# Optimization experiments

Hardware: AMD Instinct MI355X
Metric: run time of the kernel (lower is better)

## Reference

```python
import jax, jax.numpy as jnp
import numpy as np

N_NODES = 50000
N_EDGES = 800000
IN_DIM = 16
H1, H2, H3, HFC = 64, 128, 256, 256


def setup_inputs() -> dict:
    key = jax.random.key(0)
    ks = jax.random.split(key, 8)
    w = lambda k, s: jax.random.normal(k, s, dtype=jnp.float32) * 0.05
    return {
        "X": jax.random.normal(ks[0], (N_NODES, IN_DIM), dtype=jnp.float32),
        "edge_index": jax.random.randint(ks[1], (2, N_EDGES), 0, N_NODES, dtype=jnp.int64),
        "W1": w(ks[2], (2 * IN_DIM, H1)), "b1": jnp.zeros((H1,), jnp.float32),
        "W2": w(ks[3], (2 * H1, H2)), "b2": jnp.zeros((H2,), jnp.float32),
        "W3": w(ks[4], (2 * H2, H3)), "b3": jnp.zeros((H3,), jnp.float32),
        "Wf1": w(ks[5], (H3, HFC)), "bf1": jnp.zeros((HFC,), jnp.float32),
        "Wf2": w(ks[6], (HFC, 1)), "bf2": jnp.zeros((1,), jnp.float32),
    }


def edge_conv(x, edge_index, W, b):
    # EdgeConv (DGCNN): msg = ReLU(Linear([x_i, x_j - x_i])), max-aggregate at i
    src, dst = edge_index[0], edge_index[1]
    xi = x[dst]                      # [E, d] target node feats
    xj = x[src]                      # [E, d] source node feats
    msg = jax.nn.relu(jnp.concatenate([xi, xj - xi], axis=-1) @ W + b)  # [E, out]
    agg = jax.ops.segment_max(msg, dst, num_segments=x.shape[0])        # [N, out]
    # nodes with no incoming edge get -inf from segment_max -> zero them
    return jnp.where(jnp.isneginf(agg), 0.0, agg)


def reference(X, edge_index, W1, b1, W2, b2, W3, b3, Wf1, bf1, Wf2, bf2):
    H = edge_conv(X, edge_index, W1, b1)
    H = edge_conv(H, edge_index, W2, b2)
    H = edge_conv(H, edge_index, W3, b3)
    # MLP head (dropout is identity at inference)
    H = jax.nn.relu(H @ Wf1 + bf1)
    out = jax.nn.sigmoid(H @ Wf2 + bf2)
    return out.squeeze(-1)  # [N]
```

## Files before the change

kernel.cpp:

```cpp
#include <hip/hip_runtime.h>
#include <math.h>

#define NN 50000
#define NE 800000

typedef unsigned short ushort_t;
typedef __attribute__((ext_vector_type(8))) short bf16x8;
typedef __attribute__((ext_vector_type(4))) float f32x4;

__device__ inline unsigned short f2bf(float f) {
    unsigned int u = __float_as_uint(f);
    u = (u + 0x7fffu + ((u >> 16) & 1u)) >> 16;
    return (unsigned short)u;
}
__device__ inline unsigned int pack2bf(float lo, float hi) {
    return (unsigned int)f2bf(lo) | ((unsigned int)f2bf(hi) << 16);
}

__global__ void prep0_kernel(const int* __restrict__ ei, int istride,
                             int* __restrict__ esrc32, int* __restrict__ edst32,
                             int* __restrict__ deg) {
    int i = blockIdx.x * blockDim.x + threadIdx.x;
    int s = gridDim.x * blockDim.x;
    for (int j = i; j < NN; j += s) deg[j] = 0;
    const int* eis = ei;
    const int* eid = ei + (size_t)NE * istride;
    for (int j = i; j < NE; j += s) {
        esrc32[j] = eis[(size_t)j * istride];
        edst32[j] = eid[(size_t)j * istride];
    }
}

__global__ void hist_kernel(const int* __restrict__ edst, int* __restrict__ deg, int nE) {
    int i = blockIdx.x * blockDim.x + threadIdx.x;
    int s = gridDim.x * blockDim.x;
    for (; i < nE; i += s) atomicAdd(&deg[edst[i]], 1);
}

__global__ __launch_bounds__(256)
void scan_reduce(const int* __restrict__ deg, int* __restrict__ bsum, int n) {
    __shared__ int s[256];
    const int t = threadIdx.x;
    const int i = blockIdx.x * 256 + t;
    s[t] = (i < n) ? deg[i] : 0;
    __syncthreads();
#pragma unroll
    for (int off = 128; off > 0; off >>= 1) {
        if (t < off) s[t] += s[t + off];
        __syncthreads();
    }
    if (t == 0) bsum[blockIdx.x] = s[0];
}

__global__ __launch_bounds__(256)
void scan_tops(const int* __restrict__ bsum, int* __restrict__ boff,
               int* __restrict__ rowptr, int nb, int n) {
    __shared__ int s[256];
    const int t = threadIdx.x;
    const int v = (t < nb) ? bsum[t] : 0;
    s[t] = v;
    __syncthreads();
    for (int off = 1; off < 256; off <<= 1) {
        int u = (t >= off) ? s[t - off] : 0;
        __syncthreads();
        s[t] += u;
        __syncthreads();
    }
    if (t < nb) boff[t] = s[t] - v;
    if (t == 255) rowptr[n] = s[255];
}

__global__ __launch_bounds__(256)
void scan_apply(int* __restrict__ deg, const int* __restrict__ boff,
                int* __restrict__ rowptr, int n) {
    __shared__ int s[256];
    const int t = threadIdx.x;
    const int i = blockIdx.x * 256 + t;
    const int v = (i < n) ? deg[i] : 0;
    s[t] = v;
    __syncthreads();
    for (int off = 1; off < 256; off <<= 1) {
        int u = (t >= off) ? s[t - off] : 0;
        __syncthreads();
        s[t] += u;
        __syncthreads();
    }
    if (i < n) {
        int ex = boff[blockIdx.x] + s[t] - v;
        rowptr[i] = ex;
        deg[i] = ex;
    }
}

__global__ void scatter_kernel(const int* __restrict__ esrc, const int* __restrict__ edst,
                               int* __restrict__ cursor, int* __restrict__ col, int nE) {
    int i = blockIdx.x * blockDim.x + threadIdx.x;
    int s = gridDim.x * blockDim.x;
    for (; i < nE; i += s) {
        int d = edst[i];
        int pos = atomicAdd(&cursor[d], 1);
        col[pos] = esrc[i];
    }
}

__global__ void megaprep_kernel(const float* __restrict__ W1, const float* __restrict__ W2,
                                const float* __restrict__ W3, const float* __restrict__ Wf1,
                                const float* __restrict__ X,
                                ushort_t* __restrict__ Wt1, ushort_t* __restrict__ Wt2,
                                ushort_t* __restrict__ Wt3, ushort_t* __restrict__ Wf1t,
                                ushort_t* __restrict__ Xb, float* __restrict__ hacc) {
    const int T0 = 128 * 32;
    const int T1 = T0 + 256 * 64;
    const int T2 = T1 + 512 * 128;
    const int T3 = T2 + 256 * 256;
    const int T4 = T3 + NN * 32;
    const int T5 = T4 + NN;
    int i = blockIdx.x * blockDim.x + threadIdx.x;
    int s = gridDim.x * blockDim.x;
    for (; i < T5; i += s) {
        if (i < T0) {
            int idx = i, o = idx / 32, k = idx % 32;
            float v = 0.f;
            if (k < 16)
                v = (o < 64) ? (W1[k * 64 + o] - W1[(k + 16) * 64 + o])
                             : W1[(k + 16) * 64 + (o - 64)];
            Wt1[idx] = f2bf(v);
        } else if (i < T1) {
            int idx = i - T0, o = idx / 64, k = idx % 64;
            float v = (o < 128) ? (W2[k * 128 + o] - W2[(k + 64) * 128 + o])
                                : W2[(k + 64) * 128 + (o - 128)];
            Wt2[idx] = f2bf(v);
        } else if (i < T2) {
            int idx = i - T1, o = idx / 128, k = idx % 128;
            float v = (o < 256) ? (W3[(size_t)k * 256 + o] - W3[(size_t)(k + 128) * 256 + o])
                                : W3[(size_t)(k + 128) * 256 + (o - 256)];
            Wt3[idx] = f2bf(v);
        } else if (i < T3) {
            int idx = i - T2, nn = idx / 256, k = idx % 256;
            Wf1t[idx] = f2bf(Wf1[(size_t)k * 256 + nn]);
        } else if (i < T4) {
            int idx = i - T3, row = idx >> 5, c = idx & 31;
            Xb[idx] = (c < 16) ? f2bf(X[(size_t)row * 16 + c]) : (ushort_t)0;
        } else {
            hacc[i - T4] = 0.f;
        }
    }
}

template<int K, int OUT, int NF, int MR>
__global__ __launch_bounds__(256, 3)
void gemm_mfma(const ushort_t* __restrict__ A, const ushort_t* __restrict__ Wt,
               const float* __restrict__ bias, ushort_t* __restrict__ PQ, int n) {
    constexpr int NOUT = 2 * OUT;
    constexpr int KB = K / 32;
    __shared__ ushort_t lds[128][132];

    const int wave = threadIdx.x >> 6;
    const int lane = threadIdx.x & 63;
    const int lr = lane & 15;
    const int kg = lane >> 4;
    const int row0b = blockIdx.x * (4 * MR * 16);
    const int row0 = row0b + wave * (MR * 16);
    const int col0 = blockIdx.y * (NF * 16);

    f32x4 acc[MR][NF];
#pragma unroll
    for (int m = 0; m < MR; ++m)
#pragma unroll
        for (int f = 0; f < NF; ++f) acc[m][f] = (f32x4)(0.f);

    const ushort_t* Ap[MR];
#pragma unroll
    for (int m = 0; m < MR; ++m) {
        int arow = row0 + m * 16 + lr;
        if (arow >= n) arow = n - 1;
        Ap[m] = A + (size_t)arow * K + kg * 8;
    }
    const ushort_t* Bp = Wt + (size_t)(col0 + lr) * K + kg * 8;

    bf16x8 af[2][MR];
    bf16x8 bfv[2][NF];
#pragma unroll
    for (int m = 0; m < MR; ++m) af[0][m] = *(const bf16x8*)(Ap[m]);
#pragma unroll
    for (int f = 0; f < NF; ++f) bfv[0][f] = *(const bf16x8*)(Bp + (size_t)f * 16 * K);

#pragma unroll
    for (int kb = 0; kb < KB; ++kb) {
        const int cur = kb & 1, nxt = cur ^ 1;
        if (kb + 1 < KB) {
#pragma unroll
            for (int m = 0; m < MR; ++m)
                af[nxt][m] = *(const bf16x8*)(Ap[m] + (kb + 1) * 32);
#pragma unroll
            for (int f = 0; f < NF; ++f)
                bfv[nxt][f] = *(const bf16x8*)(Bp + (size_t)f * 16 * K + (kb + 1) * 32);
        }
#pragma unroll
        for (int f = 0; f < NF; ++f)
#pragma unroll
            for (int m = 0; m < MR; ++m)
                acc[m][f] = __builtin_amdgcn_mfma_f32_16x16x32_bf16(af[cur][m], bfv[cur][f], acc[m][f], 0, 0, 0);
    }

#pragma unroll
    for (int m = 0; m < MR; ++m) {
#pragma unroll
        for (int f = 0; f < NF; ++f) {
            int cg = col0 + f * 16 + lr;
            float bb = (cg < OUT) ? bias[cg] : 0.f;
#pragma unroll
            for (int r = 0; r < 4; ++r) {
                lds[wave * (MR * 16) + m * 16 + kg * 4 + r][f * 16 + lr] =
                    f2bf(acc[m][f][r] + bb);
            }
        }
    }
    __syncthreads();

    const int t = threadIdx.x;
#pragma unroll
    for (int it = 0; it < 8; ++it) {
        int j = it * 256 + t;
        int row = j >> 4;
        int q = j & 15;
        int grow = row0b + row;
        if (grow < n) {
            uint4 v = *(const uint4*)(&lds[row][q * 8]);
            *(uint4*)(PQ + (size_t)grow * NOUT + col0 + q * 8) = v;
        }
    }
}

__global__ __launch_bounds__(256, 3)
void head_mfma(const ushort_t* __restrict__ H, const ushort_t* __restrict__ Wf1t,
               const float* __restrict__ bf1, const float* __restrict__ Wf2,
               float* __restrict__ hacc, int n) {
    __shared__ ushort_t ldsB[64 * 264];

    const int t = threadIdx.x;
    const int wave = t >> 6;
    const int lane = t & 63;
    const int lr = lane & 15;
    const int kg = lane >> 4;
    const int row0 = blockIdx.x * 256 + wave * 64;
    const int col0 = blockIdx.y * 64;

#pragma unroll
    for (int it = 0; it < 8; ++it) {
        int j = it * 256 + t;
        int row = j >> 5;
        int q = j & 31;
        uint4 v = *(const uint4*)(Wf1t + (size_t)(col0 + row) * 256 + q * 8);
        *(uint4*)(&ldsB[row * 264 + q * 8]) = v;
    }
    __syncthreads();

    f32x4 acc[4][4];
#pragma unroll
    for (int m = 0; m < 4; ++m)
#pragma unroll
        for (int f = 0; f < 4; ++f) acc[m][f] = (f32x4)(0.f);

    const ushort_t* Ap[4];
#pragma unroll
    for (int m = 0; m < 4; ++m) {
        int arow = row0 + m * 16 + lr;
        if (arow >= n) arow = n - 1;
        Ap[m] = H + (size_t)arow * 256 + kg * 8;
    }
    const ushort_t* Bl = ldsB + lr * 264 + kg * 8;

#pragma unroll
    for (int kb = 0; kb < 8; ++kb) {
        bf16x8 af[4];
#pragma unroll
        for (int m = 0; m < 4; ++m) af[m] = *(const bf16x8*)(Ap[m] + kb * 32);
        bf16x8 bfv[4];
#pragma unroll
        for (int f = 0; f < 4; ++f)
            bfv[f] = *(const bf16x8*)(Bl + f * 16 * 264 + kb * 32);
#pragma unroll
        for (int f = 0; f < 4; ++f)
#pragma unroll
            for (int m = 0; m < 4; ++m)
                acc[m][f] = __builtin_amdgcn_mfma_f32_16x16x32_bf16(af[m], bfv[f], acc[m][f], 0, 0, 0);
    }

    float part[4][4];
#pragma unroll
    for (int m = 0; m < 4; ++m)
#pragma unroll
        for (int r = 0; r < 4; ++r) part[m][r] = 0.f;

#pragma unroll
    for (int f = 0; f < 4; ++f) {
        int c = col0 + f * 16 + lr;
        float w2 = Wf2[c];
        float bb = bf1[c];
#pragma unroll
        for (int m = 0; m < 4; ++m)
#pragma unroll
            for (int r = 0; r < 4; ++r)
                part[m][r] = fmaf(fmaxf(acc[m][f][r] + bb, 0.f), w2, part[m][r]);
    }
#pragma unroll
    for (int s = 1; s < 16; s <<= 1) {
#pragma unroll
        for (int m = 0; m < 4; ++m)
#pragma unroll
            for (int r = 0; r < 4; ++r)
                part[m][r] += __shfl_xor(part[m][r], s, 16);
    }
    if (lr == 0) {
#pragma unroll
        for (int m = 0; m < 4; ++m)
#pragma unroll
            for (int r = 0; r < 4; ++r) {
                int row = row0 + m * 16 + kg * 4 + r;
                if (row < n) atomicAdd(&hacc[row], part[m][r]);
            }
    }
}

__global__ void sigmoid_kernel(const float* __restrict__ hacc, const float* __restrict__ bf2,
                               float* __restrict__ out, int n) {
    int i = blockIdx.x * blockDim.x + threadIdx.x;
    int s = gridDim.x * blockDim.x;
    float b = bf2[0];
    for (; i < n; i += s) out[i] = 1.f / (1.f + expf(-(hacc[i] + b)));
}

template<int OUT>
__global__ __launch_bounds__(256, 8)
void segmax_combine(const ushort_t* __restrict__ PQ, const int* __restrict__ rowptr,
                    const int* __restrict__ col, ushort_t* __restrict__ Hout, int n) {
    constexpr int NOUT = 2 * OUT;
    constexpr int G = OUT / 8;
    constexpr int NPB = 256 / G;
    const int gid = threadIdx.x / G;
    const int lane = threadIdx.x % G;
    const int i = blockIdx.x * NPB + gid;
    if (i >= n) return;

    const int r0 = rowptr[i];
    const int r1 = rowptr[i + 1];
    const int c8 = lane * 8;

    float m[8];
#pragma unroll
    for (int j = 0; j < 8; ++j) m[j] = -INFINITY;

    auto domax = [&](uint4 q) {
        m[0] = fmaxf(m[0], __uint_as_float(q.x << 16));
        m[1] = fmaxf(m[1], __uint_as_float(q.x & 0xffff0000u));
        m[2] = fmaxf(m[2], __uint_as_float(q.y << 16));
        m[3] = fmaxf(m[3], __uint_as_float(q.y & 0xffff0000u));
        m[4] = fmaxf(m[4], __uint_as_float(q.z << 16));
        m[5] = fmaxf(m[5], __uint_as_float(q.z & 0xffff0000u));
        m[6] = fmaxf(m[6], __uint_as_float(q.w << 16));
        m[7] = fmaxf(m[7], __uint_as_float(q.w & 0xffff0000u));
    };

    int r = r0;
    for (; r + 3 < r1; r += 4) {
        int s0 = col[r], s1 = col[r + 1], s2 = col[r + 2], s3 = col[r + 3];
        uint4 q0 = *(const uint4*)(PQ + (size_t)s0 * NOUT + OUT + c8);
        uint4 q1 = *(const uint4*)(PQ + (size_t)s1 * NOUT + OUT + c8);
        uint4 q2 = *(const uint4*)(PQ + (size_t)s2 * NOUT + OUT + c8);
        uint4 q3 = *(const uint4*)(PQ + (size_t)s3 * NOUT + OUT + c8);
        domax(q0); domax(q1); domax(q2); domax(q3);
    }
    for (; r < r1; ++r) {
        domax(*(const uint4*)(PQ + (size_t)col[r] * NOUT + OUT + c8));
    }

    const uint4 pb = *(const uint4*)(PQ + (size_t)i * NOUT + c8);
    float p[8];
    p[0] = __uint_as_float(pb.x << 16); p[1] = __uint_as_float(pb.x & 0xffff0000u);
    p[2] = __uint_as_float(pb.y << 16); p[3] = __uint_as_float(pb.y & 0xffff0000u);
    p[4] = __uint_as_float(pb.z << 16); p[5] = __uint_as_float(pb.z & 0xffff0000u);
    p[6] = __uint_as_float(pb.w << 16); p[7] = __uint_as_float(pb.w & 0xffff0000u);

    float h[8];
#pragma unroll
    for (int j = 0; j < 8; ++j) h[j] = fmaxf(p[j] + m[j], 0.f);

    uint4 o;
    o.x = pack2bf(h[0], h[1]);
    o.y = pack2bf(h[2], h[3]);
    o.z = pack2bf(h[4], h[5]);
    o.w = pack2bf(h[6], h[7]);
    *(uint4*)(Hout + (size_t)i * OUT + c8) = o;
}

extern "C" void kernel_launch(void* const* d_in, const int* in_sizes, int n_in,
                              void* d_out, int out_size, void* d_ws, size_t ws_size,
                              hipStream_t stream) {
    const float* X   = (const float*)d_in[0];
    const int*   ei  = (const int*)d_in[1];
    const float* W1  = (const float*)d_in[2];
    const float* b1  = (const float*)d_in[3];
    const float* W2  = (const float*)d_in[4];
    const float* b2  = (const float*)d_in[5];
    const float* W3  = (const float*)d_in[6];
    const float* b3  = (const float*)d_in[7];
    const float* Wf1 = (const float*)d_in[8];
    const float* bf1 = (const float*)d_in[9];
    const float* Wf2 = (const float*)d_in[10];
    const float* bf2 = (const float*)d_in[11];
    float* out = (float*)d_out;

    int istride = (in_sizes[1] == 4 * NE) ? 2 : 1;

    ushort_t* PQ     = (ushort_t*)d_ws;
    ushort_t* Ha     = PQ + (size_t)NN * 512;
    ushort_t* Hb     = Ha + (size_t)NN * 256;
    int*      rowptr = (int*)(Hb + (size_t)NN * 256);
    int*      deg    = rowptr + (NN + 8);
    int*      col    = deg + NN;
    int*      esrc32 = col + NE;
    int*      edst32 = esrc32 + NE;
    int*      bsum   = edst32 + NE;
    int*      boff   = bsum + 256;
    ushort_t* Wt1    = (ushort_t*)(boff + 256);
    ushort_t* Wt2    = Wt1 + 128 * 32;
    ushort_t* Wt3    = Wt2 + 256 * 64;
    ushort_t* Wf1t   = Wt3 + 512 * 128;
    ushort_t* Xb     = Wf1t + 256 * 256;
    float*    hacc   = (float*)(Xb + (size_t)NN * 32);

    const int NB = (NN + 255) / 256;

    prep0_kernel<<<1024, 256, 0, stream>>>(ei, istride, esrc32, edst32, deg);
    hist_kernel<<<1024, 256, 0, stream>>>(edst32, deg, NE);
    scan_reduce<<<NB, 256, 0, stream>>>(deg, bsum, NN);
    scan_tops<<<1, 256, 0, stream>>>(bsum, boff, rowptr, NB, NN);
    scan_apply<<<NB, 256, 0, stream>>>(deg, boff, rowptr, NN);
    scatter_kernel<<<1024, 256, 0, stream>>>(esrc32, edst32, deg, col, NE);

    megaprep_kernel<<<1024, 256, 0, stream>>>(W1, W2, W3, Wf1, X,
                                              Wt1, Wt2, Wt3, Wf1t, Xb, hacc);

    const int GB = (NN + 127) / 128;

    {
        dim3 g(GB, 1);
        gemm_mfma<32, 64, 8, 2><<<g, 256, 0, stream>>>(Xb, Wt1, b1, PQ, NN);
    }
    segmax_combine<64><<<(NN + 31) / 32, 256, 0, stream>>>(PQ, rowptr, col, Ha, NN);

    {
        dim3 g(GB, 2);
        gemm_mfma<64, 128, 8, 2><<<g, 256, 0, stream>>>(Ha, Wt2, b2, PQ, NN);
    }
    segmax_combine<128><<<(NN + 15) / 16, 256, 0, stream>>>(PQ, rowptr, col, Hb, NN);

    {
        dim3 g(GB, 4);
        gemm_mfma<128, 256, 8, 2><<<g, 256, 0, stream>>>(Hb, Wt3, b3, PQ, NN);
    }
    segmax_combine<256><<<(NN + 7) / 8, 256, 0, stream>>>(PQ, rowptr, col, Ha, NN);

    {
        dim3 g((NN + 255) / 256, 4);
        head_mfma<<<g, 256, 0, stream>>>(Ha, Wf1t, bf1, Wf2, hacc, NN);
    }
    sigmoid_kernel<<<64, 256, 0, stream>>>(hacc, bf2, out, NN);
}
```

Before: 310.2 us.

## Slice segment-max by feature column per XCD and partition CSR scatter by destination

The segment-max kernels now split each node's output features into 8 column slices, with the slice chosen by blockIdx modulo 8. On MI355X's 8 XCDs this means each XCD's L2 sees only one eighth of the PQ row footprint. The CSR scatter also filters edges by destination range per block-modulo-8 partition, so each XCD's atomics hit a disjoint cursor range. The cost is that every node's rowptr/col list is re-read 8 times, each scatter block scans all edges, and this relies on round-robin block-to-XCD dispatch.

```diff
diff --git a/kernel.cpp b/kernel.cpp
--- a/kernel.cpp
+++ b/kernel.cpp
@@ -92,14 +92,20 @@
     }
 }
 
-__global__ void scatter_kernel(const int* __restrict__ esrc, const int* __restrict__ edst,
-                               int* __restrict__ cursor, int* __restrict__ col, int nE) {
-    int i = blockIdx.x * blockDim.x + threadIdx.x;
-    int s = gridDim.x * blockDim.x;
-    for (; i < nE; i += s) {
+__global__ __launch_bounds__(256)
+void scatter_part(const int* __restrict__ esrc, const int* __restrict__ edst,
+                  int* __restrict__ cursor, int* __restrict__ col, int nE) {
+    const int part = blockIdx.x & 7;
+    const int nb = gridDim.x >> 3;
+    const int chunk = blockIdx.x >> 3;
+    const int lo = part * 6250;
+    const int hi = lo + 6250;
+    for (int i = chunk * 256 + threadIdx.x; i < nE; i += nb * 256) {
         int d = edst[i];
-        int pos = atomicAdd(&cursor[d], 1);
-        col[pos] = esrc[i];
+        if (d >= lo && d < hi) {
+            int pos = atomicAdd(&cursor[d], 1);
+            col[pos] = esrc[i];
+        }
     }
 }
 
@@ -333,19 +339,22 @@
 
 template<int OUT>
 __global__ __launch_bounds__(256, 8)
-void segmax_combine(const ushort_t* __restrict__ PQ, const int* __restrict__ rowptr,
-                    const int* __restrict__ col, ushort_t* __restrict__ Hout, int n) {
+void segmax_sliced(const ushort_t* __restrict__ PQ, const int* __restrict__ rowptr,
+                   const int* __restrict__ col, ushort_t* __restrict__ Hout, int n) {
     constexpr int NOUT = 2 * OUT;
-    constexpr int G = OUT / 8;
-    constexpr int NPB = 256 / G;
-    const int gid = threadIdx.x / G;
-    const int lane = threadIdx.x % G;
-    const int i = blockIdx.x * NPB + gid;
-    if (i >= n) return;
-
-    const int r0 = rowptr[i];
-    const int r1 = rowptr[i + 1];
-    const int c8 = lane * 8;
+    constexpr int CPS = OUT / 8;
+    constexpr int TPN = OUT / 64;
+    constexpr int NPB = 256 / TPN;
+    const int slice = blockIdx.x & 7;
+    const int chunk = blockIdx.x >> 3;
+    const int tid = threadIdx.x;
+    const int node = chunk * NPB + tid / TPN;
+    const int tq = tid % TPN;
+    if (node >= n) return;
+
+    const int c0 = slice * CPS + tq * 8;
+    const int r0 = rowptr[node];
+    const int r1 = rowptr[node + 1];
 
     float m[8];
 #pragma unroll
@@ -365,17 +374,17 @@
     int r = r0;
     for (; r + 3 < r1; r += 4) {
         int s0 = col[r], s1 = col[r + 1], s2 = col[r + 2], s3 = col[r + 3];
-        uint4 q0 = *(const uint4*)(PQ + (size_t)s0 * NOUT + OUT + c8);
-        uint4 q1 = *(const uint4*)(PQ + (size_t)s1 * NOUT + OUT + c8);
-        uint4 q2 = *(const uint4*)(PQ + (size_t)s2 * NOUT + OUT + c8);
-        uint4 q3 = *(const uint4*)(PQ + (size_t)s3 * NOUT + OUT + c8);
+        uint4 q0 = *(const uint4*)(PQ + (size_t)s0 * NOUT + OUT + c0);
+        uint4 q1 = *(const uint4*)(PQ + (size_t)s1 * NOUT + OUT + c0);
+        uint4 q2 = *(const uint4*)(PQ + (size_t)s2 * NOUT + OUT + c0);
+        uint4 q3 = *(const uint4*)(PQ + (size_t)s3 * NOUT + OUT + c0);
         domax(q0); domax(q1); domax(q2); domax(q3);
     }
     for (; r < r1; ++r) {
-        domax(*(const uint4*)(PQ + (size_t)col[r] * NOUT + OUT + c8));
-    }
-
-    const uint4 pb = *(const uint4*)(PQ + (size_t)i * NOUT + c8);
+        domax(*(const uint4*)(PQ + (size_t)col[r] * NOUT + OUT + c0));
+    }
+
+    const uint4 pb = *(const uint4*)(PQ + (size_t)node * NOUT + c0);
     float p[8];
     p[0] = __uint_as_float(pb.x << 16); p[1] = __uint_as_float(pb.x & 0xffff0000u);
     p[2] = __uint_as_float(pb.y << 16); p[3] = __uint_as_float(pb.y & 0xffff0000u);
@@ -391,7 +400,7 @@
     o.y = pack2bf(h[2], h[3]);
     o.z = pack2bf(h[4], h[5]);
     o.w = pack2bf(h[6], h[7]);
-    *(uint4*)(Hout + (size_t)i * OUT + c8) = o;
+    *(uint4*)(Hout + (size_t)node * OUT + c0) = o;
 }
 
 extern "C" void kernel_launch(void* const* d_in, const int* in_sizes, int n_in,
@@ -437,7 +446,7 @@
     scan_reduce<<<NB, 256, 0, stream>>>(deg, bsum, NN);
     scan_tops<<<1, 256, 0, stream>>>(bsum, boff, rowptr, NB, NN);
     scan_apply<<<NB, 256, 0, stream>>>(deg, boff, rowptr, NN);
-    scatter_kernel<<<1024, 256, 0, stream>>>(esrc32, edst32, deg, col, NE);
+    scatter_part<<<1024, 256, 0, stream>>>(esrc32, edst32, deg, col, NE);
 
     megaprep_kernel<<<1024, 256, 0, stream>>>(W1, W2, W3, Wf1, X,
                                               Wt1, Wt2, Wt3, Wf1t, Xb, hacc);
@@ -448,19 +457,19 @@
         dim3 g(GB, 1);
         gemm_mfma<32, 64, 8, 2><<<g, 256, 0, stream>>>(Xb, Wt1, b1, PQ, NN);
     }
-    segmax_combine<64><<<(NN + 31) / 32, 256, 0, stream>>>(PQ, rowptr, col, Ha, NN);
+    segmax_sliced<64><<<((NN + 255) / 256) * 8, 256, 0, stream>>>(PQ, rowptr, col, Ha, NN);
 
     {
         dim3 g(GB, 2);
         gemm_mfma<64, 128, 8, 2><<<g, 256, 0, stream>>>(Ha, Wt2, b2, PQ, NN);
     }
-    segmax_combine<128><<<(NN + 15) / 16, 256, 0, stream>>>(PQ, rowptr, col, Hb, NN);
+    segmax_sliced<128><<<((NN + 127) / 128) * 8, 256, 0, stream>>>(PQ, rowptr, col, Hb, NN);
 
     {
         dim3 g(GB, 4);
         gemm_mfma<128, 256, 8, 2><<<g, 256, 0, stream>>>(Hb, Wt3, b3, PQ, NN);
     }
-    segmax_combine<256><<<(NN + 7) / 8, 256, 0, stream>>>(PQ, rowptr, col, Ha, NN);
+    segmax_sliced<256><<<((NN + 63) / 64) * 8, 256, 0, stream>>>(PQ, rowptr, col, Ha, NN);
 
     {
         dim3 g((NN + 255) / 256, 4);
```

Measured after the change: 463.6 us. +49.4%, slower.

## Quantize gathered Q features to int8 per-column scales for segment max

Applied to the files above, without the earlier changes.

Computes per-column absolute maxima of the Q half of each GEMM output, quantizes Q to int8 in a new pass, and performs the neighbour segment-max over int8 rows before dequantizing and adding P. This cuts the random-gather bytes per edge in half compared with bf16, in exchange for an extra quantization kernel, atomics for the column max, and a loss of precision in the aggregated features. The histogram and scatter kernels also switch from grid-stride loops to one thread per edge.

```diff
diff --git a/kernel.cpp b/kernel.cpp
--- a/kernel.cpp
+++ b/kernel.cpp
@@ -16,13 +16,17 @@
 __device__ inline unsigned int pack2bf(float lo, float hi) {
     return (unsigned int)f2bf(lo) | ((unsigned int)f2bf(hi) << 16);
 }
+__device__ inline float bf2f(unsigned short u) {
+    return __uint_as_float((unsigned int)u << 16);
+}
 
 __global__ void prep0_kernel(const int* __restrict__ ei, int istride,
                              int* __restrict__ esrc32, int* __restrict__ edst32,
-                             int* __restrict__ deg) {
+                             int* __restrict__ deg, float* __restrict__ colmaxAll) {
     int i = blockIdx.x * blockDim.x + threadIdx.x;
     int s = gridDim.x * blockDim.x;
     for (int j = i; j < NN; j += s) deg[j] = 0;
+    for (int j = i; j < 768; j += s) colmaxAll[j] = 0.f;
     const int* eis = ei;
     const int* eid = ei + (size_t)NE * istride;
     for (int j = i; j < NE; j += s) {
@@ -33,8 +37,7 @@
 
 __global__ void hist_kernel(const int* __restrict__ edst, int* __restrict__ deg, int nE) {
     int i = blockIdx.x * blockDim.x + threadIdx.x;
-    int s = gridDim.x * blockDim.x;
-    for (; i < nE; i += s) atomicAdd(&deg[edst[i]], 1);
+    if (i < nE) atomicAdd(&deg[edst[i]], 1);
 }
 
 __global__ __launch_bounds__(256)
@@ -95,8 +98,7 @@
 __global__ void scatter_kernel(const int* __restrict__ esrc, const int* __restrict__ edst,
                                int* __restrict__ cursor, int* __restrict__ col, int nE) {
     int i = blockIdx.x * blockDim.x + threadIdx.x;
-    int s = gridDim.x * blockDim.x;
-    for (; i < nE; i += s) {
+    if (i < nE) {
         int d = edst[i];
         int pos = atomicAdd(&cursor[d], 1);
         col[pos] = esrc[i];
@@ -150,7 +152,8 @@
 template<int K, int OUT, int NF, int MR>
 __global__ __launch_bounds__(256, 3)
 void gemm_mfma(const ushort_t* __restrict__ A, const ushort_t* __restrict__ Wt,
-               const float* __restrict__ bias, ushort_t* __restrict__ PQ, int n) {
+               const float* __restrict__ bias, ushort_t* __restrict__ PQ,
+               float* __restrict__ colmax, int n) {
     constexpr int NOUT = 2 * OUT;
     constexpr int KB = K / 32;
     __shared__ ushort_t lds[128][132];
@@ -230,6 +233,141 @@
             *(uint4*)(PQ + (size_t)grow * NOUT + col0 + q * 8) = v;
         }
     }
+
+    if (t < 128) {
+        int cg = col0 + t;
+        if (cg >= OUT) {
+            float mx = 0.f;
+            for (int r = 0; r < 128; ++r)
+                mx = fmaxf(mx, fabsf(bf2f(lds[r][t])));
+            atomicMax((unsigned int*)&colmax[cg - OUT], __float_as_uint(mx));
+        }
+    }
+}
+
+template<int OUT>
+__global__ __launch_bounds__(256)
+void quantQ(const ushort_t* __restrict__ PQ, const float* __restrict__ colmax,
+            signed char* __restrict__ Qi, int n) {
+    constexpr int NOUT = 2 * OUT;
+    constexpr int C8 = OUT / 8;
+    int idx = blockIdx.x * 256 + threadIdx.x;
+    int s = gridDim.x * 256;
+    for (; idx < n * C8; idx += s) {
+        int row = idx / C8, c8 = (idx % C8) * 8;
+        uint4 q = *(const uint4*)(PQ + (size_t)row * NOUT + OUT + c8);
+        unsigned short us[8];
+        us[0] = q.x & 0xffff; us[1] = q.x >> 16;
+        us[2] = q.y & 0xffff; us[3] = q.y >> 16;
+        us[4] = q.z & 0xffff; us[5] = q.z >> 16;
+        us[6] = q.w & 0xffff; us[7] = q.w >> 16;
+        unsigned int out0 = 0, out1 = 0;
+#pragma unroll
+        for (int j = 0; j < 8; ++j) {
+            float cm = colmax[c8 + j];
+            float inv = cm > 0.f ? 127.f / cm : 0.f;
+            int code = (int)rintf(bf2f(us[j]) * inv);
+            code = code > 127 ? 127 : (code < -127 ? -127 : code);
+            unsigned int b = (unsigned int)(code & 0xff);
+            if (j < 4) out0 |= b << (8 * j);
+            else out1 |= b << (8 * (j - 4));
+        }
+        uint2 o; o.x = out0; o.y = out1;
+        *(uint2*)(Qi + (size_t)row * OUT + c8) = o;
+    }
+}
+
+template<int OUT, int G, int CPT>
+__global__ __launch_bounds__(256, 8)
+void segmax8(const ushort_t* __restrict__ PQ, const signed char* __restrict__ Qi,
+             const float* __restrict__ colmax, const int* __restrict__ rowptr,
+             const int* __restrict__ col, ushort_t* __restrict__ Hout, int n) {
+    constexpr int NOUT = 2 * OUT;
+    constexpr int NPB = 256 / G;
+    const int gid = threadIdx.x / G;
+    const int lane = threadIdx.x % G;
+    const int node = blockIdx.x * NPB + gid;
+    if (node >= n) return;
+
+    const int c0 = lane * CPT;
+    const int r0 = rowptr[node];
+    const int r1 = rowptr[node + 1];
+
+    int m[CPT];
+#pragma unroll
+    for (int j = 0; j < CPT; ++j) m[j] = -128;
+
+    auto bmax = [&](unsigned int w, int base) {
+#pragma unroll
+        for (int k = 0; k < 4; ++k) {
+            int b = (int)(signed char)(w >> (8 * k));
+            m[base + k] = m[base + k] > b ? m[base + k] : b;
+        }
+    };
+
+    int r = r0;
+    for (; r + 1 < r1; r += 2) {
+        int s0 = col[r], s1 = col[r + 1];
+        if constexpr (CPT == 16) {
+            uint4 a = *(const uint4*)(Qi + (size_t)s0 * OUT + c0);
+            uint4 b = *(const uint4*)(Qi + (size_t)s1 * OUT + c0);
+            bmax(a.x, 0); bmax(a.y, 4); bmax(a.z, 8); bmax(a.w, 12);
+            bmax(b.x, 0); bmax(b.y, 4); bmax(b.z, 8); bmax(b.w, 12);
+        } else {
+            uint2 a = *(const uint2*)(Qi + (size_t)s0 * OUT + c0);
+            uint2 b = *(const uint2*)(Qi + (size_t)s1 * OUT + c0);
+            bmax(a.x, 0); bmax(a.y, 4);
+            bmax(b.x, 0); bmax(b.y, 4);
+        }
+    }
+    if (r < r1) {
+        int s0 = col[r];
+        if constexpr (CPT == 16) {
+            uint4 a = *(const uint4*)(Qi + (size_t)s0 * OUT + c0);
+            bmax(a.x, 0); bmax(a.y, 4); bmax(a.z, 8); bmax(a.w, 12);
+        } else {
+            uint2 a = *(const uint2*)(Qi + (size_t)s0 * OUT + c0);
+            bmax(a.x, 0); bmax(a.y, 4);
+        }
+    }
+
+    const bool has = (r1 > r0);
+    unsigned short ps[CPT];
+    if constexpr (CPT == 16) {
+        uint4 p0 = *(const uint4*)(PQ + (size_t)node * NOUT + c0);
+        uint4 p1 = *(const uint4*)(PQ + (size_t)node * NOUT + c0 + 8);
+        ps[0] = p0.x & 0xffff; ps[1] = p0.x >> 16; ps[2] = p0.y & 0xffff; ps[3] = p0.y >> 16;
+        ps[4] = p0.z & 0xffff; ps[5] = p0.z >> 16; ps[6] = p0.w & 0xffff; ps[7] = p0.w >> 16;
+        ps[8] = p1.x & 0xffff; ps[9] = p1.x >> 16; ps[10] = p1.y & 0xffff; ps[11] = p1.y >> 16;
+        ps[12] = p1.z & 0xffff; ps[13] = p1.z >> 16; ps[14] = p1.w & 0xffff; ps[15] = p1.w >> 16;
+    } else {
+        uint4 p0 = *(const uint4*)(PQ + (size_t)node * NOUT + c0);
+        ps[0] = p0.x & 0xffff; ps[1] = p0.x >> 16; ps[2] = p0.y & 0xffff; ps[3] = p0.y >> 16;
+        ps[4] = p0.z & 0xffff; ps[5] = p0.z >> 16; ps[6] = p0.w & 0xffff; ps[7] = p0.w >> 16;
+    }
+
+    float h[CPT];
+#pragma unroll
+    for (int j = 0; j < CPT; ++j) {
+        float sc = colmax[c0 + j] * (1.f / 127.f);
+        float mv = has ? (float)m[j] * sc : -INFINITY;
+        h[j] = fmaxf(bf2f(ps[j]) + mv, 0.f);
+    }
+
+    if constexpr (CPT == 16) {
+        uint4 o0, o1;
+        o0.x = pack2bf(h[0], h[1]);  o0.y = pack2bf(h[2], h[3]);
+        o0.z = pack2bf(h[4], h[5]);  o0.w = pack2bf(h[6], h[7]);
+        o1.x = pack2bf(h[8], h[9]);  o1.y = pack2bf(h[10], h[11]);
+        o1.z = pack2bf(h[12], h[13]); o1.w = pack2bf(h[14], h[15]);
+        *(uint4*)(Hout + (size_t)node * OUT + c0) = o0;
+        *(uint4*)(Hout + (size_t)node * OUT + c0 + 8) = o1;
+    } else {
+        uint4 o0;
+        o0.x = pack2bf(h[0], h[1]); o0.y = pack2bf(h[2], h[3]);
+        o0.z = pack2bf(h[4], h[5]); o0.w = pack2bf(h[6], h[7]);
+        *(uint4*)(Hout + (size_t)node * OUT + c0) = o0;
+    }
 }
 
 __global__ __launch_bounds__(256, 3)
@@ -329,69 +467,6 @@
     int s = gridDim.x * blockDim.x;
     float b = bf2[0];
     for (; i < n; i += s) out[i] = 1.f / (1.f + expf(-(hacc[i] + b)));
-}
-
-template<int OUT>
-__global__ __launch_bounds__(256, 8)
-void segmax_combine(const ushort_t* __restrict__ PQ, const int* __restrict__ rowptr,
-                    const int* __restrict__ col, ushort_t* __restrict__ Hout, int n) {
-    constexpr int NOUT = 2 * OUT;
-    constexpr int G = OUT / 8;
-    constexpr int NPB = 256 / G;
-    const int gid = threadIdx.x / G;
-    const int lane = threadIdx.x % G;
-    const int i = blockIdx.x * NPB + gid;
-    if (i >= n) return;
-
-    const int r0 = rowptr[i];
-    const int r1 = rowptr[i + 1];
-    const int c8 = lane * 8;
-
-    float m[8];
-#pragma unroll
-    for (int j = 0; j < 8; ++j) m[j] = -INFINITY;
-
-    auto domax = [&](uint4 q) {
-        m[0] = fmaxf(m[0], __uint_as_float(q.x << 16));
-        m[1] = fmaxf(m[1], __uint_as_float(q.x & 0xffff0000u));
-        m[2] = fmaxf(m[2], __uint_as_float(q.y << 16));
-        m[3] = fmaxf(m[3], __uint_as_float(q.y & 0xffff0000u));
-        m[4] = fmaxf(m[4], __uint_as_float(q.z << 16));
-        m[5] = fmaxf(m[5], __uint_as_float(q.z & 0xffff0000u));
-        m[6] = fmaxf(m[6], __uint_as_float(q.w << 16));
-        m[7] = fmaxf(m[7], __uint_as_float(q.w & 0xffff0000u));
-    };
-
-    int r = r0;
-    for (; r + 3 < r1; r += 4) {
-        int s0 = col[r], s1 = col[r + 1], s2 = col[r + 2], s3 = col[r + 3];
-        uint4 q0 = *(const uint4*)(PQ + (size_t)s0 * NOUT + OUT + c8);
-        uint4 q1 = *(const uint4*)(PQ + (size_t)s1 * NOUT + OUT + c8);
-        uint4 q2 = *(const uint4*)(PQ + (size_t)s2 * NOUT + OUT + c8);
-        uint4 q3 = *(const uint4*)(PQ + (size_t)s3 * NOUT + OUT + c8);
-        domax(q0); domax(q1); domax(q2); domax(q3);
-    }
-    for (; r < r1; ++r) {
-        domax(*(const uint4*)(PQ + (size_t)col[r] * NOUT + OUT + c8));
-    }
-
-    const uint4 pb = *(const uint4*)(PQ + (size_t)i * NOUT + c8);
-    float p[8];
-    p[0] = __uint_as_float(pb.x << 16); p[1] = __uint_as_float(pb.x & 0xffff0000u);
-    p[2] = __uint_as_float(pb.y << 16); p[3] = __uint_as_float(pb.y & 0xffff0000u);
-    p[4] = __uint_as_float(pb.z << 16); p[5] = __uint_as_float(pb.z & 0xffff0000u);
-    p[6] = __uint_as_float(pb.w << 16); p[7] = __uint_as_float(pb.w & 0xffff0000u);
-
-    float h[8];
-#pragma unroll
-    for (int j = 0; j < 8; ++j) h[j] = fmaxf(p[j] + m[j], 0.f);
-
-    uint4 o;
-    o.x = pack2bf(h[0], h[1]);
-    o.y = pack2bf(h[2], h[3]);
-    o.z = pack2bf(h[4], h[5]);
-    o.w = pack2bf(h[6], h[7]);
-    *(uint4*)(Hout + (size_t)i * OUT + c8) = o;
 }
 
 extern "C" void kernel_launch(void* const* d_in, const int* in_sizes, int n_in,
@@ -413,31 +488,37 @@
 
     int istride = (in_sizes[1] == 4 * NE) ? 2 : 1;
 
-    ushort_t* PQ     = (ushort_t*)d_ws;
-    ushort_t* Ha     = PQ + (size_t)NN * 512;
-    ushort_t* Hb     = Ha + (size_t)NN * 256;
-    int*      rowptr = (int*)(Hb + (size_t)NN * 256);
-    int*      deg    = rowptr + (NN + 8);
-    int*      col    = deg + NN;
-    int*      esrc32 = col + NE;
-    int*      edst32 = esrc32 + NE;
-    int*      bsum   = edst32 + NE;
-    int*      boff   = bsum + 256;
-    ushort_t* Wt1    = (ushort_t*)(boff + 256);
-    ushort_t* Wt2    = Wt1 + 128 * 32;
-    ushort_t* Wt3    = Wt2 + 256 * 64;
-    ushort_t* Wf1t   = Wt3 + 512 * 128;
-    ushort_t* Xb     = Wf1t + 256 * 256;
-    float*    hacc   = (float*)(Xb + (size_t)NN * 32);
+    ushort_t*    PQ     = (ushort_t*)d_ws;
+    ushort_t*    Ha     = PQ + (size_t)NN * 512;
+    ushort_t*    Hb     = Ha + (size_t)NN * 256;
+    signed char* Qi     = (signed char*)(Hb + (size_t)NN * 256);
+    int*         rowptr = (int*)(Qi + (size_t)NN * 256);
+    int*         deg    = rowptr + (NN + 8);
+    int*         col    = deg + NN;
+    int*         esrc32 = col + NE;
+    int*         edst32 = esrc32 + NE;
+    int*         bsum   = edst32 + NE;
+    int*         boff   = bsum + 256;
+    float*       cmAll  = (float*)(boff + 256);
+    float*       cm1    = cmAll;
+    float*       cm2    = cmAll + 256;
+    float*       cm3    = cmAll + 512;
+    ushort_t*    Wt1    = (ushort_t*)(cmAll + 768);
+    ushort_t*    Wt2    = Wt1 + 128 * 32;
+    ushort_t*    Wt3    = Wt2 + 256 * 64;
+    ushort_t*    Wf1t   = Wt3 + 512 * 128;
+    ushort_t*    Xb     = Wf1t + 256 * 256;
+    float*       hacc   = (float*)(Xb + (size_t)NN * 32);
 
     const int NB = (NN + 255) / 256;
-
-    prep0_kernel<<<1024, 256, 0, stream>>>(ei, istride, esrc32, edst32, deg);
-    hist_kernel<<<1024, 256, 0, stream>>>(edst32, deg, NE);
+    const int EB = (NE + 255) / 256;
+
+    prep0_kernel<<<1024, 256, 0, stream>>>(ei, istride, esrc32, edst32, deg, cmAll);
+    hist_kernel<<<EB, 256, 0, stream>>>(edst32, deg, NE);
     scan_reduce<<<NB, 256, 0, stream>>>(deg, bsum, NN);
     scan_tops<<<1, 256, 0, stream>>>(bsum, boff, rowptr, NB, NN);
     scan_apply<<<NB, 256, 0, stream>>>(deg, boff, rowptr, NN);
-    scatter_kernel<<<1024, 256, 0, stream>>>(esrc32, edst32, deg, col, NE);
+    scatter_kernel<<<EB, 256, 0, stream>>>(esrc32, edst32, deg, col, NE);
 
     megaprep_kernel<<<1024, 256, 0, stream>>>(W1, W2, W3, Wf1, X,
                                               Wt1, Wt2, Wt3, Wf1t, Xb, hacc);
@@ -446,21 +527,24 @@
 
     {
         dim3 g(GB, 1);
-        gemm_mfma<32, 64, 8, 2><<<g, 256, 0, stream>>>(Xb, Wt1, b1, PQ, NN);
-    }
-    segmax_combine<64><<<(NN + 31) / 32, 256, 0, stream>>>(PQ, rowptr, col, Ha, NN);
+        gemm_mfma<32, 64, 8, 2><<<g, 256, 0, stream>>>(Xb, Wt1, b1, PQ, cm1, NN);
+    }
+    quantQ<64><<<1563, 256, 0, stream>>>(PQ, cm1, Qi, NN);
+    segmax8<64, 8, 8><<<(NN + 31) / 32, 256, 0, stream>>>(PQ, Qi, cm1, rowptr, col, Ha, NN);
 
     {
         dim3 g(GB, 2);
-        gemm_mfma<64, 128, 8, 2><<<g, 256, 0, stream>>>(Ha, Wt2, b2, PQ, NN);
-    }
-    segmax_combine<128><<<(NN + 15) / 16, 256, 0, stream>>>(PQ, rowptr, col, Hb, NN);
+        gemm_mfma<64, 128, 8, 2><<<g, 256, 0, stream>>>(Ha, Wt2, b2, PQ, cm2, NN);
+    }
+    quantQ<128><<<3125, 256, 0, stream>>>(PQ, cm2, Qi, NN);
+    segmax8<128, 8, 16><<<(NN + 31) / 32, 256, 0, stream>>>(PQ, Qi, cm2, rowptr, col, Hb, NN);
 
     {
         dim3 g(GB, 4);
-        gemm_mfma<128, 256, 8, 2><<<g, 256, 0, stream>>>(Hb, Wt3, b3, PQ, NN);
-    }
-    segmax_combine<256><<<(NN + 7) / 8, 256, 0, stream>>>(PQ, rowptr, col, Ha, NN);
+        gemm_mfma<128, 256, 8, 2><<<g, 256, 0, stream>>>(Hb, Wt3, b3, PQ, cm3, NN);
+    }
+    quantQ<256><<<4096, 256, 0, stream>>>(PQ, cm3, Qi, NN);
+    segmax8<256, 16, 16><<<(NN + 15) / 16, 256, 0, stream>>>(PQ, Qi, cm3, rowptr, col, Ha, NN);
 
     {
         dim3 g((NN + 255) / 256, 4);
```

After: 360.8 us. 1.16x slower.
